# Kernel optimization log

Hardware: AMD Instinct MI355X
Metric: run time of the kernel (lower is better)

The kernel has to match this reference:

```python
import jax, jax.numpy as jnp
import numpy as np

IN_FEATS = 16
OUT_FEATS = 16
EDGE_FEATS = 16
N_NODES = 50000
N_EDGES = 800000


def setup_inputs() -> dict:
    key = jax.random.key(0)
    k = jax.random.split(key, 7)
    feat = jax.random.normal(k[0], (N_NODES, IN_FEATS), dtype=jnp.float32)
    efeat = jax.random.normal(k[1], (N_EDGES, EDGE_FEATS), dtype=jnp.float32)
    # edge_nn = Linear(EDGE_FEATS, IN_FEATS*OUT_FEATS)
    We = jax.random.normal(k[2], (EDGE_FEATS, IN_FEATS * OUT_FEATS), dtype=jnp.float32) * 0.1
    be = jax.random.normal(k[3], (IN_FEATS * OUT_FEATS,), dtype=jnp.float32) * 0.1
    bias = jax.random.normal(k[4], (OUT_FEATS,), dtype=jnp.float32) * 0.1
    src = jax.random.randint(k[5], (N_EDGES,), 0, N_NODES, dtype=jnp.int64 if jax.config.jax_enable_x64 else jnp.int32)
    dst = jnp.sort(jax.random.randint(k[6], (N_EDGES,), 0, N_NODES, dtype=jnp.int64 if jax.config.jax_enable_x64 else jnp.int32))
    return {"feat": feat, "efeat": efeat, "We": We, "be": be, "bias": bias,
            "src": src, "dst": dst, "num_nodes": N_NODES}


def reference(feat, efeat, We, be, bias, src, dst, num_nodes):
    # edge-conditioned weights: [E, in, out]
    w = (efeat @ We + be).reshape(-1, IN_FEATS, OUT_FEATS)
    # gather source features and per-edge matvec: sum_i h_src[e,i] * w[e,i,o]
    m = jnp.einsum('ei,eio->eo', feat[src], w)  # [E, out]
    # segment-sum aggregation to destination nodes ('sum' reducer)
    neigh = jax.ops.segment_sum(m, dst, num_segments=num_nodes)  # [N, out]
    # residual (Identity since in_feats == out_feats) + bias
    return neigh + feat + bias
```

## Files before the change

### kernel.cpp

```cpp
#include <hip/hip_runtime.h>
#include <hip/hip_bf16.h>

typedef __attribute__((ext_vector_type(8))) short short8v;
typedef __attribute__((ext_vector_type(4))) float f32x4;

#define TPW 4

__global__ __launch_bounds__(256) void setup_kernel(
    const float* __restrict__ feat, const float* __restrict__ bias,
    const float* __restrict__ We, const float* __restrict__ be,
    float* __restrict__ out, unsigned short* __restrict__ wp,
    int n_elems, int initB) {
  if ((int)blockIdx.x < initB) {
    int g = blockIdx.x * 256 + threadIdx.x;
    int base = g * 4;
    if (base < n_elems) {
      float4 f = *reinterpret_cast<const float4*>(feat + base);
      const float4* b4 = reinterpret_cast<const float4*>(bias);
      float4 b = b4[g & 3];
      float4 o;
      o.x = f.x + b.x; o.y = f.y + b.y; o.z = f.z + b.z; o.w = f.w + b.w;
      *reinterpret_cast<float4*>(out + base) = o;
    }
  } else {
    int idx = (blockIdx.x - initB) * 256 + threadIdx.x;
    if (idx < 9 * 4 * 16 * 8) {
      int j = idx & 7, n = (idx >> 3) & 15, gg = (idx >> 7) & 3, t = idx >> 9;
      int k = t * 32 + gg * 8 + j;
      float v = 0.f;
      if (k < 256) v = We[(k >> 4) * 256 + (k & 15) * 16 + n];
      else if (k < 272) v = be[(k - 256) * 16 + n];
      __hip_bfloat16 b = __float2bfloat16(v);
      wp[idx] = __builtin_bit_cast(unsigned short, b);
    }
  }
}

__global__ __launch_bounds__(256, 4) void edge_mfma_kernel(
    const float* __restrict__ feat, const float* __restrict__ efeat,
    const int* __restrict__ src, const int* __restrict__ dst,
    const unsigned short* __restrict__ wp,
    float* __restrict__ out, int E) {
  int wave = (blockIdx.x * blockDim.x + threadIdx.x) >> 6;
  int lane = threadIdx.x & 63;
  int g = lane >> 4;
  int m = lane & 15;
  int p = g >> 1;
  int hb = (g & 1) * 8;

  short8v Bf[9];
#pragma unroll
  for (int t = 0; t < 9; ++t)
    Bf[t] = *reinterpret_cast<const short8v*>(wp + ((size_t)(t * 4 + g) * 16 + m) * 8);

  int e0 = wave * TPW * 16;
  if (e0 >= E) return;

  float4 Ea, Eb, Ec, Ed, Ha, Hb;
  int4 dd;
  {
    int e = e0 + m;
    const float4* efp = reinterpret_cast<const float4*>(efeat + (size_t)e * 16);
    Ea = efp[0]; Eb = efp[1]; Ec = efp[2]; Ed = efp[3];
    int s = src[e];
    dd = *reinterpret_cast<const int4*>(dst + e0 + g * 4);
    const float4* hp = reinterpret_cast<const float4*>(feat + (size_t)s * 16 + hb);
    Ha = hp[0]; Hb = hp[1];
  }

#pragma unroll
  for (int tt = 0; tt < TPW; ++tt) {
    int e0n = e0 + 16;
    bool hn = (tt < TPW - 1) && (e0n < E);

    float4 EaN, EbN, EcN, EdN;
    int4 ddN;
    int sN = 0;
    if (hn) {
      int en = e0n + m;
      const float4* efp = reinterpret_cast<const float4*>(efeat + (size_t)en * 16);
      EaN = efp[0]; EbN = efp[1]; EcN = efp[2]; EdN = efp[3];
      sN = src[en];
      ddN = *reinterpret_cast<const int4*>(dst + e0n + g * 4);
    }

    float h[8] = {Ha.x, Ha.y, Ha.z, Ha.w, Hb.x, Hb.y, Hb.z, Hb.w};
    float efs[8];
    efs[0] = p ? Ea.y : Ea.x;  efs[1] = p ? Ea.w : Ea.z;
    efs[2] = p ? Eb.y : Eb.x;  efs[3] = p ? Eb.w : Eb.z;
    efs[4] = p ? Ec.y : Ec.x;  efs[5] = p ? Ec.w : Ec.z;
    efs[6] = p ? Ed.y : Ed.x;  efs[7] = p ? Ed.w : Ed.z;

    f32x4 acc = {0.f, 0.f, 0.f, 0.f};
#pragma unroll
    for (int t = 0; t < 8; ++t) {
      short8v A;
#pragma unroll
      for (int jj = 0; jj < 8; ++jj) {
        float prod = efs[t] * h[jj];
        __hip_bfloat16 bb = __float2bfloat16(prod);
        A[jj] = __builtin_bit_cast(short, bb);
      }
      acc = __builtin_amdgcn_mfma_f32_16x16x32_bf16(A, Bf[t], acc, 0, 0, 0);
    }

    float4 HaN, HbN;
    if (hn) {
      const float4* hp = reinterpret_cast<const float4*>(feat + (size_t)sN * 16 + hb);
      HaN = hp[0]; HbN = hp[1];
    }

    {
      short8v A;
#pragma unroll
      for (int jj = 0; jj < 8; ++jj) {
        float hv = (g < 2) ? h[jj] : 0.f;
        __hip_bfloat16 bb = __float2bfloat16(hv);
        A[jj] = __builtin_bit_cast(short, bb);
      }
      acc = __builtin_amdgcn_mfma_f32_16x16x32_bf16(A, Bf[8], acc, 0, 0, 0);
    }

    {
      float run = acc[0];
      int cur = dd.x;
      if (dd.y == cur) run += acc[1];
      else { unsafeAtomicAdd(out + (size_t)cur * 16 + m, run); cur = dd.y; run = acc[1]; }
      if (dd.z == cur) run += acc[2];
      else { unsafeAtomicAdd(out + (size_t)cur * 16 + m, run); cur = dd.z; run = acc[2]; }
      if (dd.w == cur) run += acc[3];
      else { unsafeAtomicAdd(out + (size_t)cur * 16 + m, run); cur = dd.w; run = acc[3]; }
      unsafeAtomicAdd(out + (size_t)cur * 16 + m, run);
    }

    Ea = EaN; Eb = EbN; Ec = EcN; Ed = EdN;
    Ha = HaN; Hb = HbN;
    dd = ddN;
    e0 = e0n;
    if (!hn) break;
  }
}

extern "C" void kernel_launch(void* const* d_in, const int* in_sizes, int n_in,
                              void* d_out, int out_size, void* d_ws, size_t ws_size,
                              hipStream_t stream) {
  const float* feat  = (const float*)d_in[0];
  const float* efeat = (const float*)d_in[1];
  const float* We    = (const float*)d_in[2];
  const float* be    = (const float*)d_in[3];
  const float* bias  = (const float*)d_in[4];
  const int*   src   = (const int*)d_in[5];
  const int*   dst   = (const int*)d_in[6];
  float* out = (float*)d_out;

  int E = in_sizes[5];
  int n_elems = out_size;

  int groups = (n_elems + 3) / 4;
  int initB = (groups + 255) / 256;
  int prepB = (9 * 4 * 16 * 8 + 255) / 256;
  setup_kernel<<<initB + prepB, 256, 0, stream>>>(feat, bias, We, be, out,
                                                  (unsigned short*)d_ws, n_elems, initB);

  int tiles = (E + 15) / 16;
  int waves = (tiles + TPW - 1) / TPW;
  int blocks = (waves + 3) / 4;
  edge_mfma_kernel<<<blocks, 256, 0, stream>>>(feat, efeat, src, dst,
                                               (const unsigned short*)d_ws, out, E);
}
```

Baseline: 50.57 us.

## Hoist all tile loads upfront and halve per-lane efeat loads via weight repacking

Repacks the bf16 weight layout so that each lane needs only 8 contiguous efeat values (indexed by p) instead of all 16 followed by a select, halving efeat load traffic per lane. In the full-tile path, all src, efeat and feat gathers for the wave's four tiles are issued together before any compute, replacing the one-tile-ahead software prefetch and exposing more memory-level parallelism. A separate masked tail path handles partial tiles. The extra live registers for four tiles of inputs could raise VGPR pressure and reduce occupancy.

```diff
diff --git a/kernel.cpp b/kernel.cpp
--- a/kernel.cpp
+++ b/kernel.cpp
@@ -26,14 +26,56 @@
     int idx = (blockIdx.x - initB) * 256 + threadIdx.x;
     if (idx < 9 * 4 * 16 * 8) {
       int j = idx & 7, n = (idx >> 3) & 15, gg = (idx >> 7) & 3, t = idx >> 9;
-      int k = t * 32 + gg * 8 + j;
       float v = 0.f;
-      if (k < 256) v = We[(k >> 4) * 256 + (k & 15) * 16 + n];
-      else if (k < 272) v = be[(k - 256) * 16 + n];
+      if (t < 8) {
+        int c = (gg >> 1) * 8 + t;
+        int i = (gg & 1) * 8 + j;
+        v = We[c * 256 + i * 16 + n];
+      } else if (gg < 2) {
+        v = be[(gg * 8 + j) * 16 + n];
+      }
       __hip_bfloat16 b = __float2bfloat16(v);
       wp[idx] = __builtin_bit_cast(unsigned short, b);
     }
   }
+}
+
+__device__ __forceinline__ void tile_compute(
+    float4 E0, float4 E1, float4 H0, float4 H1, int4 dd,
+    int g, int m, const short8v* Bf, float* __restrict__ out) {
+  float efs[8] = {E0.x, E0.y, E0.z, E0.w, E1.x, E1.y, E1.z, E1.w};
+  float h[8]   = {H0.x, H0.y, H0.z, H0.w, H1.x, H1.y, H1.z, H1.w};
+  f32x4 acc = {0.f, 0.f, 0.f, 0.f};
+#pragma unroll
+  for (int t = 0; t < 8; ++t) {
+    short8v A;
+#pragma unroll
+    for (int jj = 0; jj < 8; ++jj) {
+      float prod = efs[t] * h[jj];
+      __hip_bfloat16 bb = __float2bfloat16(prod);
+      A[jj] = __builtin_bit_cast(short, bb);
+    }
+    acc = __builtin_amdgcn_mfma_f32_16x16x32_bf16(A, Bf[t], acc, 0, 0, 0);
+  }
+  {
+    short8v A;
+#pragma unroll
+    for (int jj = 0; jj < 8; ++jj) {
+      float hv = (g < 2) ? h[jj] : 0.f;
+      __hip_bfloat16 bb = __float2bfloat16(hv);
+      A[jj] = __builtin_bit_cast(short, bb);
+    }
+    acc = __builtin_amdgcn_mfma_f32_16x16x32_bf16(A, Bf[8], acc, 0, 0, 0);
+  }
+  float run = acc[0];
+  int cur = dd.x;
+  if (dd.y == cur) run += acc[1];
+  else { unsafeAtomicAdd(out + (size_t)cur * 16 + m, run); cur = dd.y; run = acc[1]; }
+  if (dd.z == cur) run += acc[2];
+  else { unsafeAtomicAdd(out + (size_t)cur * 16 + m, run); cur = dd.z; run = acc[2]; }
+  if (dd.w == cur) run += acc[3];
+  else { unsafeAtomicAdd(out + (size_t)cur * 16 + m, run); cur = dd.w; run = acc[3]; }
+  unsafeAtomicAdd(out + (size_t)cur * 16 + m, run);
 }
 
 __global__ __launch_bounds__(256, 4) void edge_mfma_kernel(
@@ -53,91 +95,57 @@
   for (int t = 0; t < 9; ++t)
     Bf[t] = *reinterpret_cast<const short8v*>(wp + ((size_t)(t * 4 + g) * 16 + m) * 8);
 
-  int e0 = wave * TPW * 16;
-  if (e0 >= E) return;
+  int wave_e0 = wave * (TPW * 16);
+  if (wave_e0 >= E) return;
 
-  float4 Ea, Eb, Ec, Ed, Ha, Hb;
-  int4 dd;
-  {
-    int e = e0 + m;
-    const float4* efp = reinterpret_cast<const float4*>(efeat + (size_t)e * 16);
-    Ea = efp[0]; Eb = efp[1]; Ec = efp[2]; Ed = efp[3];
-    int s = src[e];
-    dd = *reinterpret_cast<const int4*>(dst + e0 + g * 4);
-    const float4* hp = reinterpret_cast<const float4*>(feat + (size_t)s * 16 + hb);
-    Ha = hp[0]; Hb = hp[1];
-  }
+  if (wave_e0 + TPW * 16 <= E) {
+    int sA[TPW];
+#pragma unroll
+    for (int t = 0; t < TPW; ++t) sA[t] = src[wave_e0 + t * 16 + m];
+
+    float4 E0[TPW], E1[TPW];
+#pragma unroll
+    for (int t = 0; t < TPW; ++t) {
+      const float4* efp = reinterpret_cast<const float4*>(
+          efeat + (size_t)(wave_e0 + t * 16 + m) * 16 + p * 8);
+      E0[t] = efp[0]; E1[t] = efp[1];
+    }
+
+    float4 H0[TPW], H1[TPW];
+#pragma unroll
+    for (int t = 0; t < TPW; ++t) {
+      const float4* hp = reinterpret_cast<const float4*>(feat + (size_t)sA[t] * 16 + hb);
+      H0[t] = hp[0]; H1[t] = hp[1];
+    }
 
 #pragma unroll
-  for (int tt = 0; tt < TPW; ++tt) {
-    int e0n = e0 + 16;
-    bool hn = (tt < TPW - 1) && (e0n < E);
-
-    float4 EaN, EbN, EcN, EdN;
-    int4 ddN;
-    int sN = 0;
-    if (hn) {
-      int en = e0n + m;
-      const float4* efp = reinterpret_cast<const float4*>(efeat + (size_t)en * 16);
-      EaN = efp[0]; EbN = efp[1]; EcN = efp[2]; EdN = efp[3];
-      sN = src[en];
-      ddN = *reinterpret_cast<const int4*>(dst + e0n + g * 4);
+    for (int t = 0; t < TPW; ++t) {
+      int4 dd = *reinterpret_cast<const int4*>(dst + wave_e0 + t * 16 + g * 4);
+      tile_compute(E0[t], E1[t], H0[t], H1[t], dd, g, m, Bf, out);
     }
-
-    float h[8] = {Ha.x, Ha.y, Ha.z, Ha.w, Hb.x, Hb.y, Hb.z, Hb.w};
-    float efs[8];
-    efs[0] = p ? Ea.y : Ea.x;  efs[1] = p ? Ea.w : Ea.z;
-    efs[2] = p ? Eb.y : Eb.x;  efs[3] = p ? Eb.w : Eb.z;
-    efs[4] = p ? Ec.y : Ec.x;  efs[5] = p ? Ec.w : Ec.z;
-    efs[6] = p ? Ed.y : Ed.x;  efs[7] = p ? Ed.w : Ed.z;
-
-    f32x4 acc = {0.f, 0.f, 0.f, 0.f};
-#pragma unroll
-    for (int t = 0; t < 8; ++t) {
-      short8v A;
-#pragma unroll
-      for (int jj = 0; jj < 8; ++jj) {
-        float prod = efs[t] * h[jj];
-        __hip_bfloat16 bb = __float2bfloat16(prod);
-        A[jj] = __builtin_bit_cast(short, bb);
-      }
-      acc = __builtin_amdgcn_mfma_f32_16x16x32_bf16(A, Bf[t], acc, 0, 0, 0);
+  } else {
+#pragma unroll 1
+    for (int tt = 0; tt < TPW; ++tt) {
+      int e0 = wave_e0 + tt * 16;
+      if (e0 >= E) break;
+      int e = e0 + m;
+      float vmask = (e < E) ? 1.f : 0.f;
+      int ec = (e < E) ? e : (E - 1);
+      int s = src[ec];
+      const float4* efp = reinterpret_cast<const float4*>(efeat + (size_t)ec * 16 + p * 8);
+      float4 E0v = efp[0], E1v = efp[1];
+      E0v.x *= vmask; E0v.y *= vmask; E0v.z *= vmask; E0v.w *= vmask;
+      E1v.x *= vmask; E1v.y *= vmask; E1v.z *= vmask; E1v.w *= vmask;
+      const float4* hp = reinterpret_cast<const float4*>(feat + (size_t)s * 16 + hb);
+      float4 H0v = hp[0], H1v = hp[1];
+      int4 dd;
+      int b = e0 + g * 4;
+      dd.x = dst[min(b + 0, E - 1)];
+      dd.y = dst[min(b + 1, E - 1)];
+      dd.z = dst[min(b + 2, E - 1)];
+      dd.w = dst[min(b + 3, E - 1)];
+      tile_compute(E0v, E1v, H0v, H1v, dd, g, m, Bf, out);
     }
-
-    float4 HaN, HbN;
-    if (hn) {
-      const float4* hp = reinterpret_cast<const float4*>(feat + (size_t)sN * 16 + hb);
-      HaN = hp[0]; HbN = hp[1];
-    }
-
-    {
-      short8v A;
-#pragma unroll
-      for (int jj = 0; jj < 8; ++jj) {
-        float hv = (g < 2) ? h[jj] : 0.f;
-        __hip_bfloat16 bb = __float2bfloat16(hv);
-        A[jj] = __builtin_bit_cast(short, bb);
-      }
-      acc = __builtin_amdgcn_mfma_f32_16x16x32_bf16(A, Bf[8], acc, 0, 0, 0);
-    }
-
-    {
-      float run = acc[0];
-      int cur = dd.x;
-      if (dd.y == cur) run += acc[1];
-      else { unsafeAtomicAdd(out + (size_t)cur * 16 + m, run); cur = dd.y; run = acc[1]; }
-      if (dd.z == cur) run += acc[2];
-      else { unsafeAtomicAdd(out + (size_t)cur * 16 + m, run); cur = dd.z; run = acc[2]; }
-      if (dd.w == cur) run += acc[3];
-      else { unsafeAtomicAdd(out + (size_t)cur * 16 + m, run); cur = dd.w; run = acc[3]; }
-      unsafeAtomicAdd(out + (size_t)cur * 16 + m, run);
-    }
-
-    Ea = EaN; Eb = EbN; Ec = EcN; Ed = EdN;
-    Ha = HaN; Hb = HbN;
-    dd = ddN;
-    e0 = e0n;
-    if (!hn) break;
   }
 }
 
```

Result: slower. 52.54 us (+3.9%).
